# Kernel optimization log

Hardware: AMD Instinct MI355X
Metric: run time of the kernel (lower is better)

Reference implementation:

```python
import jax, jax.numpy as jnp
import numpy as np

VOCAB, EMBED, CONV_C, HID, LABELS = 50257, 512, 512, 1024, 128
B, S = 32, 1024

def setup_inputs() -> dict:
    key = jax.random.key(0)
    ks = jax.random.split(key, 8)
    sc = lambda d: 1.0 / np.sqrt(d)
    return {
        "token_ids": jax.random.randint(ks[0], (B, S), 0, VOCAB),
        "emb_table": jax.random.normal(ks[1], (VOCAB, EMBED), jnp.float32) * 0.02,
        "conv_w": jax.random.normal(ks[2], (CONV_C, EMBED), jnp.float32) * sc(EMBED),
        "conv_b": jnp.zeros((CONV_C,), jnp.float32),
        "dec_w1": jax.random.normal(ks[3], (CONV_C, HID), jnp.float32) * sc(CONV_C),
        "dec_b1": jnp.zeros((HID,), jnp.float32),
        "dec_w2": jax.random.normal(ks[4], (HID, LABELS), jnp.float32) * sc(HID),
        "dec_b2": jnp.zeros((LABELS,), jnp.float32),
    }

def reference(token_ids, emb_table, conv_w, conv_b, dec_w1, dec_b1, dec_w2, dec_b2):
    # Embedding lookup: [B, S, E]
    x = emb_table[token_ids]
    # DocNN encoder on a length-1 sequence = kernel-1 conv + relu (+ trivial max-over-time)
    h = jax.nn.relu(jnp.einsum('bse,ce->bsc', x, conv_w) + conv_b)  # [B,S,C]
    # MLP decoder per word
    z = jax.nn.relu(jnp.einsum('bsc,ch->bsh', h, dec_w1) + dec_b1)  # [B,S,H]
    logits = jnp.einsum('bsh,hl->bsl', z, dec_w2) + dec_b2          # [B,S,L]
    # torch.cat over dim 0 of per-word outputs -> flat [B*S, L]
    return logits.reshape(-1, logits.shape[-1])
```

## Files before the change

kernel.cpp:

```cpp
#include <hip/hip_runtime.h>

typedef __bf16 bf16;
typedef __bf16 bf16x4 __attribute__((ext_vector_type(4)));
typedef __bf16 bf16x8 __attribute__((ext_vector_type(8)));
typedef float f32x4 __attribute__((ext_vector_type(4)));

#define NROWS 32768
#define EMBED 512
#define CONV_C 512
#define HID 1024
#define LABELS 128

__device__ inline void async16(const void* g, void* l) {
  __builtin_amdgcn_global_load_lds(
      (const __attribute__((address_space(1))) void*)g,
      (__attribute__((address_space(3))) void*)l, 16, 0, 0);
}


__global__ void cvt_bf16(const float* __restrict__ in, bf16* __restrict__ out, int n) {
  int i = (blockIdx.x * blockDim.x + threadIdx.x) * 4;
  if (i >= n) return;
  float4 v = *(const float4*)(in + i);
  bf16x4 o;
  o.x = (bf16)v.x; o.y = (bf16)v.y; o.z = (bf16)v.z; o.w = (bf16)v.w;
  *(bf16x4*)(out + i) = o;
}

__global__ void transpose_cvt(const float* __restrict__ in, bf16* __restrict__ out,
                              int K, int N) {
  __shared__ float t[64][65];
  int kb = blockIdx.x * 64, nb = blockIdx.y * 64;
  for (int i = threadIdx.x; i < 4096; i += 256) {
    int r = i >> 6, c = i & 63;
    t[r][c] = in[(size_t)(kb + r) * N + nb + c];
  }
  __syncthreads();
  for (int i = threadIdx.x; i < 4096; i += 256) {
    int r = i >> 6, c = i & 63;
    out[(size_t)(nb + r) * K + kb + c] = (bf16)t[c][r];
  }
}

__global__ void gather_cvt(const int* __restrict__ tok, const float* __restrict__ emb,
                           bf16* __restrict__ xb) {
  size_t i = ((size_t)blockIdx.x * blockDim.x + threadIdx.x) * 4;
  int rid = (int)(i >> 9);
  int e = (int)(i & 511);
  int t = tok[rid];
  float4 v = *(const float4*)(emb + (size_t)t * EMBED + e);
  bf16x4 o;
  o.x = (bf16)v.x; o.y = (bf16)v.y; o.z = (bf16)v.z; o.w = (bf16)v.w;
  *(bf16x4*)(xb + i) = o;
}

template <bool RELU, bool OUTBF>
__global__ __launch_bounds__(256) void gemm_bt(const bf16* __restrict__ A,
                                               const bf16* __restrict__ Bt,
                                               const float* __restrict__ bias,
                                               void* __restrict__ out,
                                               int M, int N, int K) {
  __shared__ bf16 lA[128 * 32];
  __shared__ bf16 lB[128 * 32];
  const int tid = threadIdx.x;
  const int wave = tid >> 6, lane = tid & 63;
  const int m0 = blockIdx.x * 128, n0 = blockIdx.y * 128;
  const int wm = (wave & 1) * 64, wn = (wave >> 1) * 64;
  const int lrow = lane & 15, quad = lane >> 4;

  const f32x4 zero4 = {0.f, 0.f, 0.f, 0.f};
  f32x4 acc[4][4];
#pragma unroll
  for (int i = 0; i < 4; ++i)
#pragma unroll
    for (int j = 0; j < 4; ++j) acc[i][j] = zero4;

  const int slot0 = wave * 64 + lane;

  for (int k0 = 0; k0 < K; k0 += 32) {
#pragma unroll
    for (int c = 0; c < 2; ++c) {
      int slot = slot0 + c * 256;
      int row = slot >> 2, cs = slot & 3;
      async16(A + (size_t)(m0 + row) * K + k0 + cs * 8,
              lA + (size_t)(wave * 64 + c * 256) * 8);
      async16(Bt + (size_t)(n0 + row) * K + k0 + cs * 8,
              lB + (size_t)(wave * 64 + c * 256) * 8);
    }
    __syncthreads();

    bf16x8 a[4], b[4];
#pragma unroll
    for (int t = 0; t < 4; ++t) {
      a[t] = *(const bf16x8*)(lA + (wm + t * 16 + lrow) * 32 + quad * 8);
      b[t] = *(const bf16x8*)(lB + (wn + t * 16 + lrow) * 32 + quad * 8);
    }
#pragma unroll
    for (int mi = 0; mi < 4; ++mi)
#pragma unroll
      for (int ni = 0; ni < 4; ++ni)
        acc[mi][ni] =
            __builtin_amdgcn_mfma_f32_16x16x32_bf16(a[mi], b[ni], acc[mi][ni], 0, 0, 0);
    __syncthreads();
  }

#pragma unroll
  for (int mi = 0; mi < 4; ++mi) {
#pragma unroll
    for (int ni = 0; ni < 4; ++ni) {
      int col = n0 + wn + ni * 16 + lrow;
      float bv = bias[col];
#pragma unroll
      for (int r = 0; r < 4; ++r) {
        int row = m0 + wm + mi * 16 + quad * 4 + r;
        float v = acc[mi][ni][r] + bv;
        if (RELU) v = v > 0.f ? v : 0.f;
        if (OUTBF)
          ((bf16*)out)[(size_t)row * N + col] = (bf16)v;
        else
          ((float*)out)[(size_t)row * N + col] = v;
      }
    }
  }
}


extern "C" void kernel_launch(void* const* d_in, const int* in_sizes, int n_in,
                              void* d_out, int out_size, void* d_ws, size_t ws_size,
                              hipStream_t stream) {
  const int* tok = (const int*)d_in[0];
  const float* emb = (const float*)d_in[1];
  const float* conv_w = (const float*)d_in[2];
  const float* conv_b = (const float*)d_in[3];
  const float* w1 = (const float*)d_in[4];
  const float* b1 = (const float*)d_in[5];
  const float* w2 = (const float*)d_in[6];
  const float* b2 = (const float*)d_in[7];
  float* out = (float*)d_out;

  char* ws = (char*)d_ws;
  bf16* wt_conv = (bf16*)(ws);
  bf16* wt1 = (bf16*)(ws + 524288);
  bf16* wt2 = (bf16*)(ws + 1572864);
  bf16* xb = (bf16*)(ws + 1835008);
  bf16* h = (bf16*)(ws + 1835008 + 33554432);
  bf16* z = (bf16*)(ws + 1835008 + 2 * 33554432);

  hipLaunchKernelGGL(cvt_bf16, dim3(256), dim3(256), 0, stream,
                     conv_w, wt_conv, CONV_C * EMBED);
  hipLaunchKernelGGL(transpose_cvt, dim3(8, 16), dim3(256), 0, stream,
                     w1, wt1, CONV_C, HID);
  hipLaunchKernelGGL(transpose_cvt, dim3(16, 2), dim3(256), 0, stream,
                     w2, wt2, HID, LABELS);
  hipLaunchKernelGGL(gather_cvt, dim3(16384), dim3(256), 0, stream, tok, emb, xb);

  hipLaunchKernelGGL((gemm_bt<true, true>), dim3(NROWS / 128, CONV_C / 128), dim3(256),
                     0, stream, xb, wt_conv, conv_b, (void*)h, NROWS, CONV_C, EMBED);
  hipLaunchKernelGGL((gemm_bt<true, true>), dim3(NROWS / 128, HID / 128), dim3(256),
                     0, stream, h, wt1, b1, (void*)z, NROWS, HID, CONV_C);
  hipLaunchKernelGGL((gemm_bt<false, false>), dim3(NROWS / 128, LABELS / 128), dim3(256),
                     0, stream, z, wt2, b2, (void*)out, NROWS, LABELS, HID);
}
```

Measured before the change: 283.0 us.

## Fuse embedding gather into first GEMM, deepen K-tile, shrink final GEMM tile

Removes the separate gather and conv-weight conversion kernels. The first GEMM now loads fp32 embedding rows and conv weights straight into LDS by token index and converts them to bf16 when reading fragments. The second GEMM uses a 64-wide K tile so there are fewer barriers per block. The final GEMM, with N=128, uses a 64-row M tile so twice as many blocks are launched. The trade-offs are double the LDS traffic for fp32 tiles in GEMM1 and larger LDS use in GEMM2.

```diff
diff --git a/kernel.cpp b/kernel.cpp
--- a/kernel.cpp
+++ b/kernel.cpp
@@ -17,14 +17,13 @@
       (__attribute__((address_space(3))) void*)l, 16, 0, 0);
 }
 
-
-__global__ void cvt_bf16(const float* __restrict__ in, bf16* __restrict__ out, int n) {
-  int i = (blockIdx.x * blockDim.x + threadIdx.x) * 4;
-  if (i >= n) return;
-  float4 v = *(const float4*)(in + i);
-  bf16x4 o;
-  o.x = (bf16)v.x; o.y = (bf16)v.y; o.z = (bf16)v.z; o.w = (bf16)v.w;
-  *(bf16x4*)(out + i) = o;
+__device__ inline bf16x8 cvt8(const float* p) {
+  f32x4 lo = *(const f32x4*)p;
+  f32x4 hi = *(const f32x4*)(p + 4);
+  bf16x8 r;
+  r[0] = (bf16)lo[0]; r[1] = (bf16)lo[1]; r[2] = (bf16)lo[2]; r[3] = (bf16)lo[3];
+  r[4] = (bf16)hi[0]; r[5] = (bf16)hi[1]; r[6] = (bf16)hi[2]; r[7] = (bf16)hi[3];
+  return r;
 }
 
 __global__ void transpose_cvt(const float* __restrict__ in, bf16* __restrict__ out,
@@ -42,31 +41,91 @@
   }
 }
 
-__global__ void gather_cvt(const int* __restrict__ tok, const float* __restrict__ emb,
-                           bf16* __restrict__ xb) {
-  size_t i = ((size_t)blockIdx.x * blockDim.x + threadIdx.x) * 4;
-  int rid = (int)(i >> 9);
-  int e = (int)(i & 511);
-  int t = tok[rid];
-  float4 v = *(const float4*)(emb + (size_t)t * EMBED + e);
-  bf16x4 o;
-  o.x = (bf16)v.x; o.y = (bf16)v.y; o.z = (bf16)v.z; o.w = (bf16)v.w;
-  *(bf16x4*)(xb + i) = o;
-}
-
-template <bool RELU, bool OUTBF>
+__global__ __launch_bounds__(256) void gemm1_gather(
+    const int* __restrict__ tok, const float* __restrict__ emb,
+    const float* __restrict__ convw, const float* __restrict__ bias,
+    bf16* __restrict__ out, int M, int N, int K) {
+  __shared__ __attribute__((aligned(16))) float lAf[128 * 32];
+  __shared__ __attribute__((aligned(16))) float lBf[128 * 32];
+  const int tid = threadIdx.x;
+  const int wave = tid >> 6, lane = tid & 63;
+  const int m0 = blockIdx.x * 128, n0 = blockIdx.y * 128;
+  const int wm = (wave & 1) * 64, wn = (wave >> 1) * 64;
+  const int lrow = lane & 15, quad = lane >> 4;
+  const int slot0 = wave * 64 + lane;
+  const int cs4 = (slot0 & 7) * 4;
+  const int rbase = slot0 >> 3;
+
+  int trow[4];
+#pragma unroll
+  for (int c = 0; c < 4; ++c) trow[c] = tok[m0 + rbase + c * 32];
+
+  const f32x4 zero4 = {0.f, 0.f, 0.f, 0.f};
+  f32x4 acc[4][4];
+#pragma unroll
+  for (int i = 0; i < 4; ++i)
+#pragma unroll
+    for (int j = 0; j < 4; ++j) acc[i][j] = zero4;
+
+  for (int k0 = 0; k0 < K; k0 += 32) {
+#pragma unroll
+    for (int c = 0; c < 4; ++c) {
+      int row = rbase + c * 32;
+      async16(emb + (size_t)trow[c] * EMBED + k0 + cs4,
+              lAf + (size_t)(wave * 64 + c * 256) * 4);
+      async16(convw + (size_t)(n0 + row) * K + k0 + cs4,
+              lBf + (size_t)(wave * 64 + c * 256) * 4);
+    }
+    __syncthreads();
+
+    bf16x8 a[4], b[4];
+#pragma unroll
+    for (int t = 0; t < 4; ++t) {
+      a[t] = cvt8(lAf + (wm + t * 16 + lrow) * 32 + quad * 8);
+      b[t] = cvt8(lBf + (wn + t * 16 + lrow) * 32 + quad * 8);
+    }
+#pragma unroll
+    for (int mi = 0; mi < 4; ++mi)
+#pragma unroll
+      for (int ni = 0; ni < 4; ++ni)
+        acc[mi][ni] =
+            __builtin_amdgcn_mfma_f32_16x16x32_bf16(a[mi], b[ni], acc[mi][ni], 0, 0, 0);
+    __syncthreads();
+  }
+
+#pragma unroll
+  for (int mi = 0; mi < 4; ++mi) {
+#pragma unroll
+    for (int ni = 0; ni < 4; ++ni) {
+      int col = n0 + wn + ni * 16 + lrow;
+      float bv = bias[col];
+#pragma unroll
+      for (int r = 0; r < 4; ++r) {
+        int row = m0 + wm + mi * 16 + quad * 4 + r;
+        float v = acc[mi][ni][r] + bv;
+        v = v > 0.f ? v : 0.f;
+        out[(size_t)row * N + col] = (bf16)v;
+      }
+    }
+  }
+}
+
+template <int BK, bool RELU, bool OUTBF>
 __global__ __launch_bounds__(256) void gemm_bt(const bf16* __restrict__ A,
                                                const bf16* __restrict__ Bt,
                                                const float* __restrict__ bias,
                                                void* __restrict__ out,
                                                int M, int N, int K) {
-  __shared__ bf16 lA[128 * 32];
-  __shared__ bf16 lB[128 * 32];
+  constexpr int GR = BK / 8;
+  constexpr int ISS = 128 * GR / 256;
+  __shared__ __attribute__((aligned(16))) bf16 lA[128 * BK];
+  __shared__ __attribute__((aligned(16))) bf16 lB[128 * BK];
   const int tid = threadIdx.x;
   const int wave = tid >> 6, lane = tid & 63;
   const int m0 = blockIdx.x * 128, n0 = blockIdx.y * 128;
   const int wm = (wave & 1) * 64, wn = (wave >> 1) * 64;
   const int lrow = lane & 15, quad = lane >> 4;
+  const int slot0 = wave * 64 + lane;
 
   const f32x4 zero4 = {0.f, 0.f, 0.f, 0.f};
   f32x4 acc[4][4];
@@ -75,13 +134,11 @@
 #pragma unroll
     for (int j = 0; j < 4; ++j) acc[i][j] = zero4;
 
-  const int slot0 = wave * 64 + lane;
-
-  for (int k0 = 0; k0 < K; k0 += 32) {
-#pragma unroll
-    for (int c = 0; c < 2; ++c) {
-      int slot = slot0 + c * 256;
-      int row = slot >> 2, cs = slot & 3;
+  for (int k0 = 0; k0 < K; k0 += BK) {
+#pragma unroll
+    for (int c = 0; c < ISS; ++c) {
+      int g = slot0 + c * 256;
+      int row = g / GR, cs = g % GR;
       async16(A + (size_t)(m0 + row) * K + k0 + cs * 8,
               lA + (size_t)(wave * 64 + c * 256) * 8);
       async16(Bt + (size_t)(n0 + row) * K + k0 + cs * 8,
@@ -89,18 +146,21 @@
     }
     __syncthreads();
 
-    bf16x8 a[4], b[4];
-#pragma unroll
-    for (int t = 0; t < 4; ++t) {
-      a[t] = *(const bf16x8*)(lA + (wm + t * 16 + lrow) * 32 + quad * 8);
-      b[t] = *(const bf16x8*)(lB + (wn + t * 16 + lrow) * 32 + quad * 8);
-    }
-#pragma unroll
-    for (int mi = 0; mi < 4; ++mi)
-#pragma unroll
-      for (int ni = 0; ni < 4; ++ni)
-        acc[mi][ni] =
-            __builtin_amdgcn_mfma_f32_16x16x32_bf16(a[mi], b[ni], acc[mi][ni], 0, 0, 0);
+#pragma unroll
+    for (int ks = 0; ks < BK / 32; ++ks) {
+      bf16x8 a[4], b[4];
+#pragma unroll
+      for (int t = 0; t < 4; ++t) {
+        a[t] = *(const bf16x8*)(lA + (wm + t * 16 + lrow) * BK + ks * 32 + quad * 8);
+        b[t] = *(const bf16x8*)(lB + (wn + t * 16 + lrow) * BK + ks * 32 + quad * 8);
+      }
+#pragma unroll
+      for (int mi = 0; mi < 4; ++mi)
+#pragma unroll
+        for (int ni = 0; ni < 4; ++ni)
+          acc[mi][ni] =
+              __builtin_amdgcn_mfma_f32_16x16x32_bf16(a[mi], b[ni], acc[mi][ni], 0, 0, 0);
+    }
     __syncthreads();
   }
 
@@ -119,6 +179,73 @@
           ((bf16*)out)[(size_t)row * N + col] = (bf16)v;
         else
           ((float*)out)[(size_t)row * N + col] = v;
+      }
+    }
+  }
+}
+
+__global__ __launch_bounds__(256) void gemm_bt64(const bf16* __restrict__ A,
+                                                 const bf16* __restrict__ Bt,
+                                                 const float* __restrict__ bias,
+                                                 float* __restrict__ out,
+                                                 int M, int N, int K) {
+  __shared__ __attribute__((aligned(16))) bf16 lA[64 * 32];
+  __shared__ __attribute__((aligned(16))) bf16 lB[128 * 32];
+  const int tid = threadIdx.x;
+  const int wave = tid >> 6, lane = tid & 63;
+  const int m0 = blockIdx.x * 64, n0 = 0;
+  const int wm = (wave & 1) * 32, wn = (wave >> 1) * 64;
+  const int lrow = lane & 15, quad = lane >> 4;
+  const int slot0 = wave * 64 + lane;
+
+  const f32x4 zero4 = {0.f, 0.f, 0.f, 0.f};
+  f32x4 acc[2][4];
+#pragma unroll
+  for (int i = 0; i < 2; ++i)
+#pragma unroll
+    for (int j = 0; j < 4; ++j) acc[i][j] = zero4;
+
+  for (int k0 = 0; k0 < K; k0 += 32) {
+    {
+      int row = slot0 >> 2, cs = slot0 & 3;
+      async16(A + (size_t)(m0 + row) * K + k0 + cs * 8,
+              lA + (size_t)(wave * 64) * 8);
+    }
+#pragma unroll
+    for (int c = 0; c < 2; ++c) {
+      int g = slot0 + c * 256;
+      int row = g >> 2, cs = g & 3;
+      async16(Bt + (size_t)(n0 + row) * K + k0 + cs * 8,
+              lB + (size_t)(wave * 64 + c * 256) * 8);
+    }
+    __syncthreads();
+
+    bf16x8 a[2], b[4];
+#pragma unroll
+    for (int t = 0; t < 2; ++t)
+      a[t] = *(const bf16x8*)(lA + (wm + t * 16 + lrow) * 32 + quad * 8);
+#pragma unroll
+    for (int t = 0; t < 4; ++t)
+      b[t] = *(const bf16x8*)(lB + (wn + t * 16 + lrow) * 32 + quad * 8);
+#pragma unroll
+    for (int mi = 0; mi < 2; ++mi)
+#pragma unroll
+      for (int ni = 0; ni < 4; ++ni)
+        acc[mi][ni] =
+            __builtin_amdgcn_mfma_f32_16x16x32_bf16(a[mi], b[ni], acc[mi][ni], 0, 0, 0);
+    __syncthreads();
+  }
+
+#pragma unroll
+  for (int mi = 0; mi < 2; ++mi) {
+#pragma unroll
+    for (int ni = 0; ni < 4; ++ni) {
+      int col = n0 + wn + ni * 16 + lrow;
+      float bv = bias[col];
+#pragma unroll
+      for (int r = 0; r < 4; ++r) {
+        int row = m0 + wm + mi * 16 + quad * 4 + r;
+        out[(size_t)row * N + col] = acc[mi][ni][r] + bv;
       }
     }
   }
@@ -139,25 +266,20 @@
   float* out = (float*)d_out;
 
   char* ws = (char*)d_ws;
-  bf16* wt_conv = (bf16*)(ws);
-  bf16* wt1 = (bf16*)(ws + 524288);
-  bf16* wt2 = (bf16*)(ws + 1572864);
-  bf16* xb = (bf16*)(ws + 1835008);
-  bf16* h = (bf16*)(ws + 1835008 + 33554432);
-  bf16* z = (bf16*)(ws + 1835008 + 2 * 33554432);
-
-  hipLaunchKernelGGL(cvt_bf16, dim3(256), dim3(256), 0, stream,
-                     conv_w, wt_conv, CONV_C * EMBED);
+  bf16* wt1 = (bf16*)(ws);
+  bf16* wt2 = (bf16*)(ws + (1u << 20));
+  bf16* h = (bf16*)(ws + (2u << 20));
+  bf16* z = (bf16*)(ws + (34u << 20));
+
   hipLaunchKernelGGL(transpose_cvt, dim3(8, 16), dim3(256), 0, stream,
                      w1, wt1, CONV_C, HID);
   hipLaunchKernelGGL(transpose_cvt, dim3(16, 2), dim3(256), 0, stream,
                      w2, wt2, HID, LABELS);
-  hipLaunchKernelGGL(gather_cvt, dim3(16384), dim3(256), 0, stream, tok, emb, xb);
-
-  hipLaunchKernelGGL((gemm_bt<true, true>), dim3(NROWS / 128, CONV_C / 128), dim3(256),
-                     0, stream, xb, wt_conv, conv_b, (void*)h, NROWS, CONV_C, EMBED);
-  hipLaunchKernelGGL((gemm_bt<true, true>), dim3(NROWS / 128, HID / 128), dim3(256),
+
+  hipLaunchKernelGGL(gemm1_gather, dim3(NROWS / 128, CONV_C / 128), dim3(256),
+                     0, stream, tok, emb, conv_w, conv_b, h, NROWS, CONV_C, EMBED);
+  hipLaunchKernelGGL((gemm_bt<64, true, true>), dim3(NROWS / 128, HID / 128), dim3(256),
                      0, stream, h, wt1, b1, (void*)z, NROWS, HID, CONV_C);
-  hipLaunchKernelGGL((gemm_bt<false, false>), dim3(NROWS / 128, LABELS / 128), dim3(256),
-                     0, stream, z, wt2, b2, (void*)out, NROWS, LABELS, HID);
-}
+  hipLaunchKernelGGL(gemm_bt64, dim3(NROWS / 64, 1), dim3(256),
+                     0, stream, z, wt2, b2, out, NROWS, LABELS, HID);
+}
```

Result: slower. 290.6 us (+2.7%).
